# Optimization experiments

Measured on AMD Instinct MI355X. Metric: run time of the kernel, lower is better.

Reference implementation:

```python
import jax, jax.numpy as jnp
import numpy as np

B, L, D = 32, 4096, 768
WINDOW = 32
LN_EPS = 1e-5


def setup_inputs() -> dict:
    key = jax.random.key(0)
    k1, k2, k3 = jax.random.split(key, 3)
    ref_repr = jax.random.normal(k1, (B, L, D), dtype=jnp.float32)
    alt_repr = jax.random.normal(k2, (B, L, D), dtype=jnp.float32)
    variant_pos = jax.random.randint(k3, (B,), 0, L, dtype=jnp.int64)
    gamma = jnp.ones((D,), dtype=jnp.float32)
    beta = jnp.zeros((D,), dtype=jnp.float32)
    return {"ref_repr": ref_repr, "alt_repr": alt_repr, "variant_pos": variant_pos,
            "gamma": gamma, "beta": beta}


def reference(ref_repr, alt_repr, variant_pos, gamma, beta):
    b, l, d = ref_repr.shape
    w = WINDOW
    offs = jnp.arange(-w, w + 1)                      # [2w+1]
    idx = variant_pos[:, None] + offs[None, :]        # [B, 2w+1] raw window indices
    valid = (idx >= 0) & (idx < l)                    # boundary mask (clamped window)
    idx_c = jnp.clip(idx, 0, l - 1)
    bidx = jnp.arange(b)[:, None]
    # gather only the windows, not the full sequence: [B, 2w+1, D]
    diff = alt_repr[bidx, idx_c] - ref_repr[bidx, idx_c]
    m = valid[..., None].astype(diff.dtype)
    count = valid.sum(axis=1, keepdims=True).astype(diff.dtype)  # [B,1]
    pooled = (diff * m).sum(axis=1) / count           # [B, D] masked mean over window
    # LayerNorm over D (biased variance, like nn.LayerNorm)
    mu = pooled.mean(axis=-1, keepdims=True)
    var = jnp.mean((pooled - mu) ** 2, axis=-1, keepdims=True)
    return (pooled - mu) * jax.lax.rsqrt(var + LN_EPS) * gamma + beta
```

## Files before the change

kernel.cpp:

```cpp
#include <hip/hip_runtime.h>

#define BATCH 32
#define SEQL 4096
#define DIM 768
#define D4 192
#define WIN 32
#define NPOS 65
#define CHUNKS 13
#define PERCHUNK 5
#define LN_EPS 1e-5f

__global__ __launch_bounds__(D4) void pool_partial_kernel(
    const float4* __restrict__ refv, const float4* __restrict__ altv,
    const int* __restrict__ pos, float4* __restrict__ wsv) {
  const int b = blockIdx.y;
  const int chunk = blockIdx.x;
  const int tid = threadIdx.x;
  const int p0 = pos[b] - WIN + chunk * PERCHUNK;

  float4 acc = make_float4(0.f, 0.f, 0.f, 0.f);
#pragma unroll
  for (int i = 0; i < PERCHUNK; ++i) {
    const int p = p0 + i;
    if (p >= 0 && p < SEQL) {
      const size_t off = ((size_t)b * SEQL + p) * D4 + tid;
      const float4 a = altv[off];
      const float4 r = refv[off];
      acc.x += a.x - r.x;
      acc.y += a.y - r.y;
      acc.z += a.z - r.z;
      acc.w += a.w - r.w;
    }
  }
  wsv[((size_t)b * CHUNKS + chunk) * D4 + tid] = acc;
}

__global__ __launch_bounds__(D4) void ln_kernel(
    const float4* __restrict__ wsv, const int* __restrict__ pos,
    const float4* __restrict__ gammav, const float4* __restrict__ betav,
    float4* __restrict__ outv) {
  const int b = blockIdx.x;
  const int tid = threadIdx.x;

  const int p = pos[b];
  const int lo = (p - WIN) > 0 ? (p - WIN) : 0;
  const int hi = (p + WIN) < (SEQL - 1) ? (p + WIN) : (SEQL - 1);
  const float inv_cnt = 1.f / (float)(hi - lo + 1);

  float4 s = make_float4(0.f, 0.f, 0.f, 0.f);
#pragma unroll
  for (int c = 0; c < CHUNKS; ++c) {
    const float4 v = wsv[((size_t)b * CHUNKS + c) * D4 + tid];
    s.x += v.x; s.y += v.y; s.z += v.z; s.w += v.w;
  }
  s.x *= inv_cnt; s.y *= inv_cnt; s.z *= inv_cnt; s.w *= inv_cnt;

  float lsum = s.x + s.y + s.z + s.w;
  float lsq  = s.x * s.x + s.y * s.y + s.z * s.z + s.w * s.w;

#pragma unroll
  for (int off = 32; off > 0; off >>= 1) {
    lsum += __shfl_down(lsum, off);
    lsq  += __shfl_down(lsq, off);
  }

  __shared__ float sh[6];
  const int wave = tid >> 6;
  if ((tid & 63) == 0) {
    sh[wave] = lsum;
    sh[3 + wave] = lsq;
  }
  __syncthreads();

  const float tot   = sh[0] + sh[1] + sh[2];
  const float totsq = sh[3] + sh[4] + sh[5];
  const float mu  = tot * (1.f / (float)DIM);
  const float var = totsq * (1.f / (float)DIM) - mu * mu;
  const float rstd = rsqrtf(var + LN_EPS);

  const float4 g  = gammav[tid];
  const float4 bb = betav[tid];
  float4 o;
  o.x = (s.x - mu) * rstd * g.x + bb.x;
  o.y = (s.y - mu) * rstd * g.y + bb.y;
  o.z = (s.z - mu) * rstd * g.z + bb.z;
  o.w = (s.w - mu) * rstd * g.w + bb.w;
  outv[(size_t)b * D4 + tid] = o;
}

extern "C" void kernel_launch(void* const* d_in, const int* in_sizes, int n_in,
                              void* d_out, int out_size, void* d_ws, size_t ws_size,
                              hipStream_t stream) {
  const float* ref_repr = (const float*)d_in[0];
  const float* alt_repr = (const float*)d_in[1];
  const int*   vpos     = (const int*)d_in[2];
  const float* gamma    = (const float*)d_in[3];
  const float* beta     = (const float*)d_in[4];
  float* out = (float*)d_out;
  float* ws  = (float*)d_ws;

  dim3 gridA(CHUNKS, BATCH);
  pool_partial_kernel<<<gridA, D4, 0, stream>>>(
      (const float4*)ref_repr, (const float4*)alt_repr, vpos, (float4*)ws);

  ln_kernel<<<BATCH, D4, 0, stream>>>(
      (const float4*)ws, vpos, (const float4*)gamma, (const float4*)beta,
      (float4*)out);
}
```

Baseline: 588.9 us.

## Fuse window pooling and LayerNorm into one kernel per batch row

Replaces the two-kernel scheme (chunked partial sums written to a workspace, then a LayerNorm kernel) with a single kernel that runs one block of 960 threads per batch row. Five slices of threads each sum every fifth window position; the slices are reduced in shared memory, then LayerNorm runs inside the same block. This removes the second launch and the workspace write and read-back. In exchange the grid shrinks from 416 blocks to 32, so fewer compute units share the window loads.

Result: no change. 589.4 us (+0.1%).

```diff
diff --git a/kernel.cpp b/kernel.cpp
--- a/kernel.cpp
+++ b/kernel.cpp
@@ -6,24 +6,32 @@
 #define D4 192
 #define WIN 32
 #define NPOS 65
-#define CHUNKS 13
-#define PERCHUNK 5
+#define SLICES 5
+#define PERSLICE 13
+#define NT (SLICES * D4)
 #define LN_EPS 1e-5f
 
-__global__ __launch_bounds__(D4) void pool_partial_kernel(
+__global__ __launch_bounds__(NT) void fused_vdp_kernel(
     const float4* __restrict__ refv, const float4* __restrict__ altv,
-    const int* __restrict__ pos, float4* __restrict__ wsv) {
-  const int b = blockIdx.y;
-  const int chunk = blockIdx.x;
+    const int* __restrict__ pos, const float4* __restrict__ gammav,
+    const float4* __restrict__ betav, float4* __restrict__ outv) {
+  const int b = blockIdx.x;
   const int tid = threadIdx.x;
-  const int p0 = pos[b] - WIN + chunk * PERCHUNK;
+  const int slice = tid / D4;
+  const int d4 = tid % D4;
+
+  const int p = pos[b];
+  const int p0 = p - WIN;
+  const int lo = p0 > 0 ? p0 : 0;
+  const int hi = (p + WIN) < (SEQL - 1) ? (p + WIN) : (SEQL - 1);
+  const float inv_cnt = 1.f / (float)(hi - lo + 1);
 
   float4 acc = make_float4(0.f, 0.f, 0.f, 0.f);
 #pragma unroll
-  for (int i = 0; i < PERCHUNK; ++i) {
-    const int p = p0 + i;
-    if (p >= 0 && p < SEQL) {
-      const size_t off = ((size_t)b * SEQL + p) * D4 + tid;
+  for (int k = 0; k < PERSLICE; ++k) {
+    const int q = p0 + slice + SLICES * k;
+    if (q >= 0 && q < SEQL) {
+      const size_t off = ((size_t)b * SEQL + q) * D4 + d4;
       const float4 a = altv[off];
       const float4 r = refv[off];
       acc.x += a.x - r.x;
@@ -32,60 +40,54 @@
       acc.w += a.w - r.w;
     }
   }
-  wsv[((size_t)b * CHUNKS + chunk) * D4 + tid] = acc;
-}
 
-__global__ __launch_bounds__(D4) void ln_kernel(
-    const float4* __restrict__ wsv, const int* __restrict__ pos,
-    const float4* __restrict__ gammav, const float4* __restrict__ betav,
-    float4* __restrict__ outv) {
-  const int b = blockIdx.x;
-  const int tid = threadIdx.x;
+  __shared__ float4 part[SLICES][D4];
+  __shared__ float sh[6];
+  part[slice][d4] = acc;
+  __syncthreads();
 
-  const int p = pos[b];
-  const int lo = (p - WIN) > 0 ? (p - WIN) : 0;
-  const int hi = (p + WIN) < (SEQL - 1) ? (p + WIN) : (SEQL - 1);
-  const float inv_cnt = 1.f / (float)(hi - lo + 1);
+  if (tid < D4) {
+    float4 s = part[0][tid];
+#pragma unroll
+    for (int j = 1; j < SLICES; ++j) {
+      const float4 v = part[j][tid];
+      s.x += v.x; s.y += v.y; s.z += v.z; s.w += v.w;
+    }
+    s.x *= inv_cnt; s.y *= inv_cnt; s.z *= inv_cnt; s.w *= inv_cnt;
 
-  float4 s = make_float4(0.f, 0.f, 0.f, 0.f);
+    float lsum = s.x + s.y + s.z + s.w;
+    float lsq  = s.x * s.x + s.y * s.y + s.z * s.z + s.w * s.w;
 #pragma unroll
-  for (int c = 0; c < CHUNKS; ++c) {
-    const float4 v = wsv[((size_t)b * CHUNKS + c) * D4 + tid];
-    s.x += v.x; s.y += v.y; s.z += v.z; s.w += v.w;
-  }
-  s.x *= inv_cnt; s.y *= inv_cnt; s.z *= inv_cnt; s.w *= inv_cnt;
-
-  float lsum = s.x + s.y + s.z + s.w;
-  float lsq  = s.x * s.x + s.y * s.y + s.z * s.z + s.w * s.w;
-
-#pragma unroll
-  for (int off = 32; off > 0; off >>= 1) {
-    lsum += __shfl_down(lsum, off);
-    lsq  += __shfl_down(lsq, off);
-  }
-
-  __shared__ float sh[6];
-  const int wave = tid >> 6;
-  if ((tid & 63) == 0) {
-    sh[wave] = lsum;
-    sh[3 + wave] = lsq;
+    for (int off = 32; off > 0; off >>= 1) {
+      lsum += __shfl_down(lsum, off);
+      lsq  += __shfl_down(lsq, off);
+    }
+    const int wave = tid >> 6;
+    if ((tid & 63) == 0) {
+      sh[wave] = lsum;
+      sh[3 + wave] = lsq;
+    }
+    part[0][tid] = s;
   }
   __syncthreads();
 
-  const float tot   = sh[0] + sh[1] + sh[2];
-  const float totsq = sh[3] + sh[4] + sh[5];
-  const float mu  = tot * (1.f / (float)DIM);
-  const float var = totsq * (1.f / (float)DIM) - mu * mu;
-  const float rstd = rsqrtf(var + LN_EPS);
+  if (tid < D4) {
+    const float4 s = part[0][tid];
+    const float tot   = sh[0] + sh[1] + sh[2];
+    const float totsq = sh[3] + sh[4] + sh[5];
+    const float mu  = tot * (1.f / (float)DIM);
+    const float var = totsq * (1.f / (float)DIM) - mu * mu;
+    const float rstd = rsqrtf(var + LN_EPS);
 
-  const float4 g  = gammav[tid];
-  const float4 bb = betav[tid];
-  float4 o;
-  o.x = (s.x - mu) * rstd * g.x + bb.x;
-  o.y = (s.y - mu) * rstd * g.y + bb.y;
-  o.z = (s.z - mu) * rstd * g.z + bb.z;
-  o.w = (s.w - mu) * rstd * g.w + bb.w;
-  outv[(size_t)b * D4 + tid] = o;
+    const float4 g  = gammav[tid];
+    const float4 bb = betav[tid];
+    float4 o;
+    o.x = (s.x - mu) * rstd * g.x + bb.x;
+    o.y = (s.y - mu) * rstd * g.y + bb.y;
+    o.z = (s.z - mu) * rstd * g.z + bb.z;
+    o.w = (s.w - mu) * rstd * g.w + bb.w;
+    outv[(size_t)b * D4 + tid] = o;
+  }
 }
 
 extern "C" void kernel_launch(void* const* d_in, const int* in_sizes, int n_in,
@@ -97,13 +99,8 @@
   const float* gamma    = (const float*)d_in[3];
   const float* beta     = (const float*)d_in[4];
   float* out = (float*)d_out;
-  float* ws  = (float*)d_ws;
 
-  dim3 gridA(CHUNKS, BATCH);
-  pool_partial_kernel<<<gridA, D4, 0, stream>>>(
-      (const float4*)ref_repr, (const float4*)alt_repr, vpos, (float4*)ws);
-
-  ln_kernel<<<BATCH, D4, 0, stream>>>(
-      (const float4*)ws, vpos, (const float4*)gamma, (const float4*)beta,
-      (float4*)out);
+  fused_vdp_kernel<<<BATCH, NT, 0, stream>>>(
+      (const float4*)ref_repr, (const float4*)alt_repr, vpos,
+      (const float4*)gamma, (const float4*)beta, (float4*)out);
 }
```
